# Kernel tuning notes

Hardware: AMD Instinct MI355X
Metric: run time of the kernel (lower is better)

## Reference

```python
import jax, jax.numpy as jnp
import numpy as np

N, L, IN, H1, H2, OUT = 256, 2048, 8, 256, 128, 1


def setup_inputs() -> dict:
    key = jax.random.key(0)
    ks = jax.random.split(key, 9)
    s1 = 1.0 / np.sqrt(H1)  # torch LSTMCell/Linear init scale
    s2 = 1.0 / np.sqrt(H2)
    u = lambda k, shape, s: jax.random.uniform(k, shape, jnp.float32, -s, s)
    return {
        "x": jax.random.normal(ks[0], (N, L, IN), jnp.float32),
        "W_ih": u(ks[1], (4 * H1, IN + 1), s1),
        "W_hh": u(ks[2], (4 * H1, H1), s1),
        "b_ih": u(ks[3], (4 * H1,), s1),
        "b_hh": u(ks[4], (4 * H1,), s1),
        "W1": u(ks[5], (H2, H1), s1),
        "b1": u(ks[6], (H2,), s1),
        "W2": u(ks[7], (OUT, H2), s2),
        "b2": u(ks[8], (OUT,), s2),
    }


def reference(x, W_ih, W_hh, b_ih, b_hh, W1, b1, W2, b2):
    # Dropout is identity at inference (eval mode); initial_output = 0.
    n = x.shape[0]
    h0 = jnp.zeros((n, H1), x.dtype)
    c0 = jnp.zeros((n, H1), x.dtype)
    p0 = jnp.zeros((n, OUT), x.dtype)  # prev_output

    def step(carry, x_t):
        hx, cx, prev = carry
        inp_t = jnp.concatenate([x_t, prev], axis=-1)          # [N, IN+1]
        gates = inp_t @ W_ih.T + b_ih + hx @ W_hh.T + b_hh     # [N, 4*H1]
        i, f, g, o = jnp.split(gates, 4, axis=-1)              # torch gate order i,f,g,o
        i = jax.nn.sigmoid(i)
        f = jax.nn.sigmoid(f)
        g = jnp.tanh(g)
        o = jax.nn.sigmoid(o)
        cx = f * cx + i * g
        hx = o * jnp.tanh(cx)
        out = jax.nn.relu(hx @ W1.T + b1) @ W2.T + b2          # [N, OUT]
        return (hx, cx, out), (out, cx)

    _, (outs, cells) = jax.lax.scan(step, (h0, c0, p0), jnp.swapaxes(x, 0, 1))
    output = jnp.swapaxes(outs, 0, 1)       # [N, L, OUT]
    cell_states = jnp.swapaxes(cells, 0, 1)  # [N, L, H1]
    return (output, cell_states)
```

## Files before the change

kernel.cpp:

```cpp
#include <hip/hip_runtime.h>


typedef __attribute__((ext_vector_type(8))) short short8;
typedef __attribute__((ext_vector_type(4))) float f32x4;
typedef __attribute__((ext_vector_type(2))) float f32x2;

#define LSEQ 2048

__device__ __forceinline__ unsigned short f2bf(float f) {
  unsigned int u = __float_as_uint(f);
  return (unsigned short)((u + 0x7FFFu + ((u >> 16) & 1u)) >> 16);
}
__device__ __forceinline__ float sigm(float x) {
  float e = __builtin_amdgcn_exp2f(-1.44269504089f * x);
  return __builtin_amdgcn_rcpf(1.0f + e);
}
__device__ __forceinline__ float tanh_(float x) {
  float ax = __builtin_fabsf(x);
  float e = __builtin_amdgcn_exp2f(-2.88539008178f * ax);
  float t = (1.0f - e) * __builtin_amdgcn_rcpf(1.0f + e);
  return __builtin_copysignf(t, x);
}
__device__ __forceinline__ void wg_barrier() {
  __asm__ __volatile__("s_waitcnt lgkmcnt(0)" ::: "memory");
  __builtin_amdgcn_s_barrier();
}

__global__ void prep_kernel(const float* __restrict__ W_ih, const float* __restrict__ W_hh,
                            const float* __restrict__ b_ih, const float* __restrict__ b_hh,
                            const float* __restrict__ W1,
                            unsigned short* __restrict__ wstream,
                            unsigned short* __restrict__ w1stream,
                            float* __restrict__ bias,
                            unsigned int* __restrict__ flags) {
  int tid = blockIdx.x * 256 + threadIdx.x;
  if (tid < 36864) {
    int f = tid >> 6, l = tid & 63;
    int w = f / 72, rem = f % 72, nt = rem / 9, kt = rem % 9;
    int g = (nt >> 1) * 256 + w * 32 + (nt & 1) * 16 + (l & 15);
    int k0 = kt * 32 + (l >> 4) * 8;
    unsigned short* dst = wstream + (size_t)f * 512 + l * 8;
#pragma unroll
    for (int j = 0; j < 8; j++) {
      int k = k0 + j;
      float v;
      if (k < 256)       v = W_hh[g * 256 + k];
      else if (k < 264)  v = W_ih[g * 9 + (k - 256)];
      else               v = 0.0f;
      dst[j] = f2bf(v);
    }
  } else if (tid < 36864 + 4096) {
    int t2 = tid - 36864;
    int f = t2 >> 6, l = t2 & 63;
    int w = f >> 3, kt = f & 7;
    int h2 = w * 16 + (l & 15);
    int k0 = kt * 32 + (l >> 4) * 8;
    unsigned short* dst = w1stream + (size_t)f * 512 + l * 8;
#pragma unroll
    for (int j = 0; j < 8; j++) dst[j] = f2bf(W1[h2 * 256 + k0 + j]);
  } else if (tid < 36864 + 4096 + 1024) {
    int g = tid - 36864 - 4096;
    bias[g] = b_ih[g] + b_hh[g];
  } else if (tid < 36864 + 4096 + 1024 + 2048) {
    flags[tid - 36864 - 4096 - 1024] = 0u;
  }
}

__global__ __launch_bounds__(512, 2) void lstm_main(
    const float* __restrict__ x, const float* __restrict__ W_ih,
    const float* __restrict__ b1, const float* __restrict__ W2, const float* __restrict__ b2,
    const unsigned short* __restrict__ wstream, const unsigned short* __restrict__ w1stream,
    const float* __restrict__ bias,
    unsigned short* __restrict__ packets, unsigned int* __restrict__ flags,
    float* __restrict__ out0, float* __restrict__ out1) {
  __shared__ unsigned short A[2][16][296];
  __shared__ float gbuf[4][16][34];
  __shared__ unsigned short hout[16][40];
  __shared__ float part[8][17];
  __shared__ float olds[16];

  const int tid = threadIdx.x;
  const int w = tid >> 6, l = tid & 63, lr = l & 15, lg = l >> 4;
  const int bg = blockIdx.x & 15, sl = blockIdx.x >> 4;
  const int n0 = bg * 16, u0 = sl * 32;

  short8 wg_[9], w1_[8];
  {
    const short8* wp = (const short8*)wstream;
    const short8* w1p = (const short8*)w1stream;
#pragma unroll
    for (int kt = 0; kt < 9; kt++) wg_[kt] = wp[(size_t)((sl * 8 + w) * 9 + kt) * 64 + l];
#pragma unroll
    for (int kt = 0; kt < 8; kt++) w1_[kt] = w1p[(size_t)(w * 8 + kt) * 64 + l];
  }
  const float biasv = bias[(w >> 1) * 256 + u0 + (w & 1) * 16 + lr];
  const float b1v = b1[w * 16 + lr];
  const float w2v = W2[w * 16 + lr];
  const float b2v = b2[0];

  int cs = 0, cu2 = 0;
  float wpv[8];
  float c0r = 0.f, c1r = 0.f;
  if (w >= 4) {
    int idx = tid - 256;
    cs = idx >> 4; cu2 = (idx & 15) * 2;
#pragma unroll
    for (int g = 0; g < 4; g++) {
      wpv[g * 2 + 0] = W_ih[(g * 256 + u0 + cu2) * 9 + 8];
      wpv[g * 2 + 1] = W_ih[(g * 256 + u0 + cu2 + 1) * 9 + 8];
    }
  }

  for (int i = tid; i < 2 * 16 * 296; i += 512) ((unsigned short*)A)[i] = 0;
  if (tid < 16) olds[tid] = 0.f;

  unsigned int* fl = flags + bg * 128;
  unsigned int* ownfl = fl + sl * 16;

  __syncthreads();

  for (int k = 0; k <= LSEQ; k++) {
    const int slot = k & 1;

    if (w == 1 && l < 32 && k < LSEQ) {
      f32x4 xv = *(const f32x4*)(x + ((size_t)(n0 + (l >> 1)) * LSEQ + k) * 8 + (l & 1) * 4);
      unsigned short* ax = &A[slot][l >> 1][256 + (l & 1) * 4];
      ax[0] = f2bf(xv.x); ax[1] = f2bf(xv.y); ax[2] = f2bf(xv.z); ax[3] = f2bf(xv.w);
    }
    if (k > 0 && w != sl) {
      while (__hip_atomic_load(&fl[w * 16], __ATOMIC_RELAXED, __HIP_MEMORY_SCOPE_AGENT) < (unsigned)k) {}
      __asm__ __volatile__("" ::: "memory");
      const unsigned long long* pk =
          (const unsigned long long*)(packets + (((size_t)slot * 16 + bg) * 8 + w) * 512);
      unsigned long long d0 = __hip_atomic_load(&pk[l * 2],     __ATOMIC_RELAXED, __HIP_MEMORY_SCOPE_AGENT);
      unsigned long long d1 = __hip_atomic_load(&pk[l * 2 + 1], __ATOMIC_RELAXED, __HIP_MEMORY_SCOPE_AGENT);
      unsigned long long* dst = (unsigned long long*)&A[slot][l >> 2][w * 32 + (l & 3) * 8];
      dst[0] = d0; dst[1] = d1;
    }
    wg_barrier();

    short8 afr[9];
#pragma unroll
    for (int kt = 0; kt < 9; kt++)
      afr[kt] = *(const short8*)&A[slot][lr][kt * 32 + lg * 8];
    if (k < LSEQ) {
      f32x4 acc = {biasv, biasv, biasv, biasv};
#pragma unroll
      for (int kt = 0; kt < 9; kt++)
        acc = __builtin_amdgcn_mfma_f32_16x16x32_bf16(afr[kt], wg_[kt], acc, 0, 0, 0);
#pragma unroll
      for (int r = 0; r < 4; r++) gbuf[w >> 1][lg * 4 + r][(w & 1) * 16 + lr] = acc[r];
    }
    if (k > 0) {
      f32x4 m = {b1v, b1v, b1v, b1v};
#pragma unroll
      for (int kt = 0; kt < 8; kt++)
        m = __builtin_amdgcn_mfma_f32_16x16x32_bf16(afr[kt], w1_[kt], m, 0, 0, 0);
      float p[4];
#pragma unroll
      for (int r = 0; r < 4; r++) {
        float v = m[r] > 0.f ? m[r] : 0.f;
        p[r] = v * w2v;
        p[r] += __shfl_xor(p[r], 1, 64);
        p[r] += __shfl_xor(p[r], 2, 64);
        p[r] += __shfl_xor(p[r], 4, 64);
        p[r] += __shfl_xor(p[r], 8, 64);
      }
      if (lr == 0) {
#pragma unroll
        for (int r = 0; r < 4; r++) part[w][lg * 4 + r] = p[r];
      }
    }
    wg_barrier();

    if (k > 0 && w == 3 && l < 16) {
      float o = b2v;
#pragma unroll
      for (int i = 0; i < 8; i++) o += part[i][l];
      olds[l] = o;
      if (sl == 0) __builtin_nontemporal_store(o, out0 + (size_t)(n0 + l) * LSEQ + (k - 1));
    }
    wg_barrier();

    if (k < LSEQ && w >= 4) {
      float o = olds[cs];
      float gi0 = gbuf[0][cs][cu2] + wpv[0] * o, gi1 = gbuf[0][cs][cu2 + 1] + wpv[1] * o;
      float gf0 = gbuf[1][cs][cu2] + wpv[2] * o, gf1 = gbuf[1][cs][cu2 + 1] + wpv[3] * o;
      float gg0 = gbuf[2][cs][cu2] + wpv[4] * o, gg1 = gbuf[2][cs][cu2 + 1] + wpv[5] * o;
      float go0 = gbuf[3][cs][cu2] + wpv[6] * o, go1 = gbuf[3][cs][cu2 + 1] + wpv[7] * o;
      c0r = sigm(gf0) * c0r + sigm(gi0) * tanh_(gg0);
      c1r = sigm(gf1) * c1r + sigm(gi1) * tanh_(gg1);
      float h0 = sigm(go0) * tanh_(c0r);
      float h1 = sigm(go1) * tanh_(c1r);
      f32x2 cv = {c0r, c1r};
      __builtin_nontemporal_store(cv, (f32x2*)(out1 + ((size_t)(n0 + cs) * LSEQ + k) * 256 + u0 + cu2));
      hout[cs][cu2] = f2bf(h0); hout[cs][cu2 + 1] = f2bf(h1);
      unsigned short* an = &A[slot ^ 1][cs][u0 + cu2];
      an[0] = f2bf(h0); an[1] = f2bf(h1);
    }
    wg_barrier();

    if (k < LSEQ && w == 0) {
      short8 hv = *(const short8*)&hout[l >> 2][(l & 3) * 8];
      unsigned long long* pk =
          (unsigned long long*)(packets + (((size_t)((k + 1) & 1) * 16 + bg) * 8 + sl) * 512);
      const unsigned long long* s64 = (const unsigned long long*)&hv;
      __hip_atomic_store(&pk[l * 2],     s64[0], __ATOMIC_RELAXED, __HIP_MEMORY_SCOPE_AGENT);
      __hip_atomic_store(&pk[l * 2 + 1], s64[1], __ATOMIC_RELAXED, __HIP_MEMORY_SCOPE_AGENT);
      __asm__ __volatile__("s_waitcnt vmcnt(0)" ::: "memory");
      if (l == 0)
        __hip_atomic_store(ownfl, (unsigned)(k + 1), __ATOMIC_RELAXED, __HIP_MEMORY_SCOPE_AGENT);
    }
  }
}

extern "C" void kernel_launch(void* const* d_in, const int* in_sizes, int n_in,
                              void* d_out, int out_size, void* d_ws, size_t ws_size,
                              hipStream_t stream) {
  const float* x    = (const float*)d_in[0];
  const float* W_ih = (const float*)d_in[1];
  const float* W_hh = (const float*)d_in[2];
  const float* b_ih = (const float*)d_in[3];
  const float* b_hh = (const float*)d_in[4];
  const float* W1   = (const float*)d_in[5];
  const float* b1   = (const float*)d_in[6];
  const float* W2   = (const float*)d_in[7];
  const float* b2   = (const float*)d_in[8];

  unsigned short* wstream  = (unsigned short*)d_ws;
  unsigned short* w1stream = (unsigned short*)((char*)d_ws + 1179648);
  float*          bias     = (float*)((char*)d_ws + 1179648 + 65536);
  unsigned short* packets  = (unsigned short*)((char*)d_ws + 1249280);
  unsigned int*   flags    = (unsigned int*)((char*)d_ws + 1249280 + 262144);

  float* out0 = (float*)d_out;
  float* out1 = out0 + 256 * LSEQ;

  prep_kernel<<<172, 256, 0, stream>>>(W_ih, W_hh, b_ih, b_hh, W1, wstream, w1stream, bias, flags);
  lstm_main<<<128, 512, 0, stream>>>(x, W_ih, b1, W2, b2, wstream, w1stream, bias, packets, flags,
                                     out0, out1);
}
```

Measured before the change: 5.524 ms.

## Replace flag handshake with step-tagged hidden-state packets and merge per-step phases

```diff
diff --git a/kernel.cpp b/kernel.cpp
--- a/kernel.cpp
+++ b/kernel.cpp
@@ -32,7 +32,7 @@
                             unsigned short* __restrict__ wstream,
                             unsigned short* __restrict__ w1stream,
                             float* __restrict__ bias,
-                            unsigned int* __restrict__ flags) {
+                            unsigned long long* __restrict__ packets) {
   int tid = blockIdx.x * 256 + threadIdx.x;
   if (tid < 36864) {
     int f = tid >> 6, l = tid & 63;
@@ -61,8 +61,8 @@
   } else if (tid < 36864 + 4096 + 1024) {
     int g = tid - 36864 - 4096;
     bias[g] = b_ih[g] + b_hh[g];
-  } else if (tid < 36864 + 4096 + 1024 + 2048) {
-    flags[tid - 36864 - 4096 - 1024] = 0u;
+  } else if (tid < 36864 + 4096 + 1024 + 65536) {
+    packets[tid - 41984] = 0ull;
   }
 }
 
@@ -71,13 +71,11 @@
     const float* __restrict__ b1, const float* __restrict__ W2, const float* __restrict__ b2,
     const unsigned short* __restrict__ wstream, const unsigned short* __restrict__ w1stream,
     const float* __restrict__ bias,
-    unsigned short* __restrict__ packets, unsigned int* __restrict__ flags,
+    unsigned long long* __restrict__ packets,
     float* __restrict__ out0, float* __restrict__ out1) {
   __shared__ unsigned short A[2][16][296];
   __shared__ float gbuf[4][16][34];
-  __shared__ unsigned short hout[16][40];
   __shared__ float part[8][17];
-  __shared__ float olds[16];
 
   const int tid = threadIdx.x;
   const int w = tid >> 6, l = tid & 63, lr = l & 15, lg = l >> 4;
@@ -98,12 +96,10 @@
   const float w2v = W2[w * 16 + lr];
   const float b2v = b2[0];
 
-  int cs = 0, cu2 = 0;
+  const int cs = tid >> 4, cu2 = (tid & 15) * 2;
   float wpv[8];
   float c0r = 0.f, c1r = 0.f;
-  if (w >= 4) {
-    int idx = tid - 256;
-    cs = idx >> 4; cu2 = (idx & 15) * 2;
+  if (tid < 256) {
 #pragma unroll
     for (int g = 0; g < 4; g++) {
       wpv[g * 2 + 0] = W_ih[(g * 256 + u0 + cu2) * 9 + 8];
@@ -112,30 +108,41 @@
   }
 
   for (int i = tid; i < 2 * 16 * 296; i += 512) ((unsigned short*)A)[i] = 0;
-  if (tid < 16) olds[tid] = 0.f;
-
-  unsigned int* fl = flags + bg * 128;
-  unsigned int* ownfl = fl + sl * 16;
+
+  f32x4 xv = {0.f, 0.f, 0.f, 0.f};
+  if (w == sl && l < 32)
+    xv = *(const f32x4*)(x + (size_t)(n0 + (l >> 1)) * LSEQ * 8 + (l & 1) * 4);
 
   __syncthreads();
 
   for (int k = 0; k <= LSEQ; k++) {
     const int slot = k & 1;
 
-    if (w == 1 && l < 32 && k < LSEQ) {
-      f32x4 xv = *(const f32x4*)(x + ((size_t)(n0 + (l >> 1)) * LSEQ + k) * 8 + (l & 1) * 4);
-      unsigned short* ax = &A[slot][l >> 1][256 + (l & 1) * 4];
-      ax[0] = f2bf(xv.x); ax[1] = f2bf(xv.y); ax[2] = f2bf(xv.z); ax[3] = f2bf(xv.w);
-    }
-    if (k > 0 && w != sl) {
-      while (__hip_atomic_load(&fl[w * 16], __ATOMIC_RELAXED, __HIP_MEMORY_SCOPE_AGENT) < (unsigned)k) {}
-      __asm__ __volatile__("" ::: "memory");
-      const unsigned long long* pk =
-          (const unsigned long long*)(packets + (((size_t)slot * 16 + bg) * 8 + w) * 512);
-      unsigned long long d0 = __hip_atomic_load(&pk[l * 2],     __ATOMIC_RELAXED, __HIP_MEMORY_SCOPE_AGENT);
-      unsigned long long d1 = __hip_atomic_load(&pk[l * 2 + 1], __ATOMIC_RELAXED, __HIP_MEMORY_SCOPE_AGENT);
-      unsigned long long* dst = (unsigned long long*)&A[slot][l >> 2][w * 32 + (l & 3) * 8];
-      dst[0] = d0; dst[1] = d1;
+    if (w == sl) {
+      if (l < 32 && k < LSEQ) {
+        unsigned long long xp = (unsigned long long)f2bf(xv.x)
+                              | ((unsigned long long)f2bf(xv.y) << 16)
+                              | ((unsigned long long)f2bf(xv.z) << 32)
+                              | ((unsigned long long)f2bf(xv.w) << 48);
+        *(unsigned long long*)&A[slot][l >> 1][256 + (l & 1) * 4] = xp;
+        if (k + 1 < LSEQ)
+          xv = *(const f32x4*)(x + ((size_t)(n0 + (l >> 1)) * LSEQ + (k + 1)) * 8 + (l & 1) * 4);
+      }
+    } else if (k > 0) {
+      const unsigned long long* pk = packets + (((size_t)slot * 16 + bg) * 8 + w) * 256 + l * 4;
+      unsigned long long v[4];
+#pragma unroll
+      for (int i = 0; i < 4; i++)
+        v[i] = __hip_atomic_load(&pk[i], __ATOMIC_RELAXED, __HIP_MEMORY_SCOPE_AGENT);
+#pragma unroll
+      for (int i = 0; i < 4; i++)
+        while ((unsigned)(v[i] & 0xFFFFu) != (unsigned)k)
+          v[i] = __hip_atomic_load(&pk[i], __ATOMIC_RELAXED, __HIP_MEMORY_SCOPE_AGENT);
+#pragma unroll
+      for (int i = 0; i < 4; i++) {
+        int W = l * 4 + i, s = W >> 4, pr = W & 15;
+        *(unsigned int*)&A[slot][s][w * 32 + pr * 2] = (unsigned int)(v[i] >> 16);
+      }
     }
     wg_barrier();
 
@@ -173,43 +180,36 @@
     }
     wg_barrier();
 
-    if (k > 0 && w == 3 && l < 16) {
-      float o = b2v;
-#pragma unroll
-      for (int i = 0; i < 8; i++) o += part[i][l];
-      olds[l] = o;
-      if (sl == 0) __builtin_nontemporal_store(o, out0 + (size_t)(n0 + l) * LSEQ + (k - 1));
-    }
-    wg_barrier();
-
-    if (k < LSEQ && w >= 4) {
-      float o = olds[cs];
-      float gi0 = gbuf[0][cs][cu2] + wpv[0] * o, gi1 = gbuf[0][cs][cu2 + 1] + wpv[1] * o;
-      float gf0 = gbuf[1][cs][cu2] + wpv[2] * o, gf1 = gbuf[1][cs][cu2 + 1] + wpv[3] * o;
-      float gg0 = gbuf[2][cs][cu2] + wpv[4] * o, gg1 = gbuf[2][cs][cu2 + 1] + wpv[5] * o;
-      float go0 = gbuf[3][cs][cu2] + wpv[6] * o, go1 = gbuf[3][cs][cu2 + 1] + wpv[7] * o;
-      c0r = sigm(gf0) * c0r + sigm(gi0) * tanh_(gg0);
-      c1r = sigm(gf1) * c1r + sigm(gi1) * tanh_(gg1);
-      float h0 = sigm(go0) * tanh_(c0r);
-      float h1 = sigm(go1) * tanh_(c1r);
-      f32x2 cv = {c0r, c1r};
-      __builtin_nontemporal_store(cv, (f32x2*)(out1 + ((size_t)(n0 + cs) * LSEQ + k) * 256 + u0 + cu2));
-      hout[cs][cu2] = f2bf(h0); hout[cs][cu2 + 1] = f2bf(h1);
-      unsigned short* an = &A[slot ^ 1][cs][u0 + cu2];
-      an[0] = f2bf(h0); an[1] = f2bf(h1);
-    }
-    wg_barrier();
-
-    if (k < LSEQ && w == 0) {
-      short8 hv = *(const short8*)&hout[l >> 2][(l & 3) * 8];
-      unsigned long long* pk =
-          (unsigned long long*)(packets + (((size_t)((k + 1) & 1) * 16 + bg) * 8 + sl) * 512);
-      const unsigned long long* s64 = (const unsigned long long*)&hv;
-      __hip_atomic_store(&pk[l * 2],     s64[0], __ATOMIC_RELAXED, __HIP_MEMORY_SCOPE_AGENT);
-      __hip_atomic_store(&pk[l * 2 + 1], s64[1], __ATOMIC_RELAXED, __HIP_MEMORY_SCOPE_AGENT);
-      __asm__ __volatile__("s_waitcnt vmcnt(0)" ::: "memory");
-      if (l == 0)
-        __hip_atomic_store(ownfl, (unsigned)(k + 1), __ATOMIC_RELAXED, __HIP_MEMORY_SCOPE_AGENT);
+    if (tid < 256) {
+      float o = 0.f;
+      if (k > 0) {
+        o = b2v;
+#pragma unroll
+        for (int i = 0; i < 8; i++) o += part[i][cs];
+        if (cu2 == 0 && sl == 0)
+          __builtin_nontemporal_store(o, out0 + (size_t)(n0 + cs) * LSEQ + (k - 1));
+      }
+      if (k < LSEQ) {
+        float gi0 = gbuf[0][cs][cu2] + wpv[0] * o, gi1 = gbuf[0][cs][cu2 + 1] + wpv[1] * o;
+        float gf0 = gbuf[1][cs][cu2] + wpv[2] * o, gf1 = gbuf[1][cs][cu2 + 1] + wpv[3] * o;
+        float gg0 = gbuf[2][cs][cu2] + wpv[4] * o, gg1 = gbuf[2][cs][cu2 + 1] + wpv[5] * o;
+        float go0 = gbuf[3][cs][cu2] + wpv[6] * o, go1 = gbuf[3][cs][cu2 + 1] + wpv[7] * o;
+        c0r = sigm(gf0) * c0r + sigm(gi0) * tanh_(gg0);
+        c1r = sigm(gf1) * c1r + sigm(gi1) * tanh_(gg1);
+        float h0 = sigm(go0) * tanh_(c0r);
+        float h1 = sigm(go1) * tanh_(c1r);
+        f32x2 cv = {c0r, c1r};
+        __builtin_nontemporal_store(cv,
+            (f32x2*)(out1 + ((size_t)(n0 + cs) * LSEQ + k) * 256 + u0 + cu2));
+        unsigned int hb0 = f2bf(h0), hb1 = f2bf(h1);
+        unsigned long long wv = (unsigned long long)(unsigned)(k + 1)
+                              | ((unsigned long long)hb0 << 16)
+                              | ((unsigned long long)hb1 << 32);
+        unsigned long long* dst =
+            packets + (((size_t)((k + 1) & 1) * 16 + bg) * 8 + sl) * 256 + tid;
+        __hip_atomic_store(dst, wv, __ATOMIC_RELAXED, __HIP_MEMORY_SCOPE_AGENT);
+        *(unsigned int*)&A[slot ^ 1][cs][u0 + cu2] = hb0 | (hb1 << 16);
+      }
     }
   }
 }
@@ -227,16 +227,15 @@
   const float* W2   = (const float*)d_in[7];
   const float* b2   = (const float*)d_in[8];
 
-  unsigned short* wstream  = (unsigned short*)d_ws;
-  unsigned short* w1stream = (unsigned short*)((char*)d_ws + 1179648);
-  float*          bias     = (float*)((char*)d_ws + 1179648 + 65536);
-  unsigned short* packets  = (unsigned short*)((char*)d_ws + 1249280);
-  unsigned int*   flags    = (unsigned int*)((char*)d_ws + 1249280 + 262144);
+  unsigned short*     wstream  = (unsigned short*)d_ws;
+  unsigned short*     w1stream = (unsigned short*)((char*)d_ws + 1179648);
+  float*              bias     = (float*)((char*)d_ws + 1179648 + 65536);
+  unsigned long long* packets  = (unsigned long long*)((char*)d_ws + 1249280);
 
   float* out0 = (float*)d_out;
   float* out1 = out0 + 256 * LSEQ;
 
-  prep_kernel<<<172, 256, 0, stream>>>(W_ih, W_hh, b_ih, b_hh, W1, wstream, w1stream, bias, flags);
-  lstm_main<<<128, 512, 0, stream>>>(x, W_ih, b1, W2, b2, wstream, w1stream, bias, packets, flags,
+  prep_kernel<<<420, 256, 0, stream>>>(W_ih, W_hh, b_ih, b_hh, W1, wstream, w1stream, bias, packets);
+  lstm_main<<<128, 512, 0, stream>>>(x, W_ih, b1, W2, b2, wstream, w1stream, bias, packets,
                                      out0, out1);
 }
```

Result: slower. 5.940 ms (+7.5%).
